# Kernel tuning notes

Hardware: AMD Instinct MI355X
Metric: run time of the kernel (lower is better)

The kernel has to match this reference:

```python
import jax, jax.numpy as jnp
import numpy as np

EMBED_DIM = 512
NUM_HEADS = 8
WINDOW = 64
FFN_RATIO = 4


def _mha(q_in, kv_in, w_in, b_in, w_out, b_out, n_heads, mask=None):
    # Faithful torch.nn.MultiheadAttention (batch_first) with packed in_proj.
    b, sq, d = q_in.shape
    sk = kv_in.shape[1]
    hd = d // n_heads
    wq, wk, wv = jnp.split(w_in, 3, axis=0)   # each [d, d]
    bq, bk, bv = jnp.split(b_in, 3, axis=0)
    q = (q_in @ wq.T + bq).reshape(b, sq, n_heads, hd).transpose(0, 2, 1, 3)
    k = (kv_in @ wk.T + bk).reshape(b, sk, n_heads, hd).transpose(0, 2, 1, 3)
    v = (kv_in @ wv.T + bv).reshape(b, sk, n_heads, hd).transpose(0, 2, 1, 3)
    scores = jnp.einsum('bhqd,bhkd->bhqk', q, k) / jnp.sqrt(jnp.asarray(hd, q.dtype))
    if mask is not None:
        scores = scores + mask  # additive -inf mask, broadcast over [b, h]
    attn = jax.nn.softmax(scores, axis=-1)
    out = jnp.einsum('bhqk,bhkd->bhqd', attn, v)
    out = out.transpose(0, 2, 1, 3).reshape(b, sq, d)
    return out @ w_out.T + b_out


def _layernorm(x, g, b, eps=1e-5):
    mu = jnp.mean(x, axis=-1, keepdims=True)
    var = jnp.var(x, axis=-1, keepdims=True)
    return (x - mu) * jax.lax.rsqrt(var + eps) * g + b


def _local_causal_mask(p, window, dtype=jnp.float32):
    # row i attends to columns [max(0, i-window), i]
    i = jnp.arange(p)[:, None]
    j = jnp.arange(p)[None, :]
    allowed = (j <= i) & (j >= i - window)
    return jnp.where(allowed, jnp.zeros((), dtype), jnp.asarray(-jnp.inf, dtype))


def setup_inputs() -> dict:
    key = jax.random.key(0)
    ks = jax.random.split(key, 20)
    d, h = EMBED_DIM, EMBED_DIM * FFN_RATIO
    s = 0.02
    return {
        'x': jax.random.normal(ks[0], (64, 512, d), jnp.float32),
        'anchors': jax.random.normal(ks[1], (64, 32, d), jnp.float32),
        'lw_in': jax.random.normal(ks[2], (3 * d, d), jnp.float32) * s,
        'lb_in': jnp.zeros((3 * d,), jnp.float32),
        'lw_out': jax.random.normal(ks[3], (d, d), jnp.float32) * s,
        'lb_out': jnp.zeros((d,), jnp.float32),
        'gw_in': jax.random.normal(ks[4], (3 * d, d), jnp.float32) * s,
        'gb_in': jnp.zeros((3 * d,), jnp.float32),
        'gw_out': jax.random.normal(ks[5], (d, d), jnp.float32) * s,
        'gb_out': jnp.zeros((d,), jnp.float32),
        'w1': jax.random.normal(ks[6], (h, d), jnp.float32) * s,
        'b1': jnp.zeros((h,), jnp.float32),
        'w2': jax.random.normal(ks[7], (d, h), jnp.float32) * s,
        'b2': jnp.zeros((d,), jnp.float32),
        'g1': jnp.ones((d,), jnp.float32),
        'be1': jnp.zeros((d,), jnp.float32),
        'g2': jnp.ones((d,), jnp.float32),
        'be2': jnp.zeros((d,), jnp.float32),
    }


def reference(x, anchors, lw_in, lb_in, lw_out, lb_out, gw_in, gb_in, gw_out, gb_out,
              w1, b1, w2, b2, g1, be1, g2, be2):
    p = x.shape[1]
    mask = _local_causal_mask(p, WINDOW, x.dtype)
    x = x + _mha(x, x, lw_in, lb_in, lw_out, lb_out, NUM_HEADS, mask)
    x = x + _mha(x, anchors, gw_in, gb_in, gw_out, gb_out, NUM_HEADS)
    x = _layernorm(x, g1, be1)
    h = jax.nn.gelu(x @ w1.T + b1, approximate=False)
    ffn = h @ w2.T + b2
    return _layernorm(x + ffn, g2, be2)
```

## Files before the change

kernel.cpp:

```cpp
#include <hip/hip_runtime.h>
#include <cmath>


typedef unsigned short u16;
typedef unsigned int u32;
typedef __bf16 bf16_t;
typedef bf16_t bf16x8 __attribute__((ext_vector_type(8)));
typedef float f32x4 __attribute__((ext_vector_type(4)));

#define DEV __device__ __forceinline__
#define MFMA16(a, b, c) __builtin_amdgcn_mfma_f32_16x16x32_bf16(a, b, c, 0, 0, 0)
#define SBAR() __builtin_amdgcn_sched_barrier(0)

DEV u16 f2b(float f) {
  u32 u = __float_as_uint(f);
  u32 r = u + 0x7fffu + ((u >> 16) & 1u);
  return (u16)(r >> 16);
}
DEV float b2f(u16 b) { return __uint_as_float(((u32)b) << 16); }

DEV float gelu_erf(float x) {
  float y = x * 0.70710678118654752f;
  float ay = fabsf(y);
  float t = __builtin_amdgcn_rcpf(1.0f + 0.3275911f * ay);
  float p = t * (0.254829592f +
            t * (-0.284496736f +
            t * (1.421413741f +
            t * (-1.453152027f + t * 1.061405429f))));
  float e = 1.0f - p * __expf(-y * y);
  float erfv = (y < 0.f) ? -e : e;
  return 0.5f * x * (1.0f + erfv);
}

DEV void g2l16(const void* g, void* l) {
  __builtin_amdgcn_global_load_lds((const __attribute__((address_space(1))) void*)g,
                                   (__attribute__((address_space(3))) void*)l,
                                   16, 0, 0);
}

__global__ __launch_bounds__(256) void conv1(const float* __restrict__ s,
                                             u16* __restrict__ d) {
  size_t idx = ((size_t)blockIdx.x * 256 + threadIdx.x) * 8;
  float4 a = *(const float4*)(s + idx);
  float4 b = *(const float4*)(s + idx + 4);
  float v[8] = {a.x, a.y, a.z, a.w, b.x, b.y, b.z, b.w};
  union { u16 q[8]; uint4 u; } pk;
#pragma unroll
  for (int i = 0; i < 8; ++i) pk.q[i] = f2b(v[i]);
  *(uint4*)(d + idx) = pk.u;
}

template <bool GELU, bool RES32, bool RESB, bool OUT32, bool OUTB>
__global__ __launch_bounds__(512, 4) void gemm128(
    const u16* __restrict__ A, const u16* __restrict__ B,
    const float* __restrict__ bias, const float* __restrict__ res32,
    const u16* __restrict__ resb, float* __restrict__ out32,
    u16* __restrict__ outb, int M, int N, int K) {
  __shared__ __align__(16) char smem[73728];
  const int tid = threadIdx.x;
  const int lane = tid & 63, wv = tid >> 6;
  const int warp_m = wv >> 2, warp_n = wv & 3;
  const int lrow = lane & 15, quad = lane >> 4;

  int idx = blockIdx.x;
  {
    const int nwg = gridDim.x;
    if (nwg >= 8) {
      const int q = nwg >> 3, r = nwg & 7;
      const int xcd = idx & 7, rk = idx >> 3;
      idx = (xcd < r ? xcd * (q + 1) : r * (q + 1) + (xcd - r) * q) + rk;
    }
  }
  const int nx = N >> 8;
  const int m0 = (idx / nx) * 128, n0 = (idx % nx) * 256;

  const int srow = tid >> 2;
  const int scol = (((tid & 3) ^ ((tid >> 3) & 3)) << 4);
  const int sdst = tid * 16;
  const int cs = (quad * 16) ^ (((lrow >> 1) & 3) << 4);
  const int rdA = warp_m * 4096 + lrow * 64 + cs;
  const int rdB = warp_n * 4096 + lrow * 64 + cs;

  const int nt = K >> 5;

  auto stage3 = [&](int kt, int slot) {
    const char* ga = (const char*)A + (((size_t)(m0 + srow) * K + kt * 32) << 1) + scol;
    g2l16(ga, smem + slot * 8192 + sdst);
    const char* gb = (const char*)B + (((size_t)(n0 + srow) * K + kt * 32) << 1) + scol;
    char* lb = smem + 24576 + slot * 16384 + sdst;
    g2l16(gb, lb);
    g2l16(gb + ((size_t)K << 8), lb + 8192);
  };

  f32x4 acc[4][4];
  f32x4 zero4 = {0.f, 0.f, 0.f, 0.f};
#pragma unroll
  for (int a = 0; a < 4; ++a)
#pragma unroll
    for (int b = 0; b < 4; ++b) acc[a][b] = zero4;

  stage3(0, 0);
  stage3(1, 1);
  SBAR();
  asm volatile("s_waitcnt vmcnt(3)" ::: "memory");
  asm volatile("s_barrier" ::: "memory");
  SBAR();

  int c0s = 0, c2s = 2;
  for (int kt = 0; kt < nt; ++kt) {
    const char* cA = smem + c0s * 8192;
    const char* cB = smem + 24576 + c0s * 16384;
    bf16x8 afr[4], bfr[4];
#pragma unroll
    for (int m = 0; m < 4; ++m) afr[m] = *(const bf16x8*)(cA + rdA + m * 1024);
#pragma unroll
    for (int n = 0; n < 4; ++n) bfr[n] = *(const bf16x8*)(cB + rdB + n * 1024);
    const int kt2 = (kt + 2 < nt) ? kt + 2 : nt - 1;
    stage3(kt2, c2s);
    SBAR();
    asm volatile("s_barrier" ::: "memory");
    asm volatile("s_waitcnt lgkmcnt(0)" ::: "memory");
    SBAR();
    __builtin_amdgcn_s_setprio(1);
#pragma unroll
    for (int m = 0; m < 4; ++m)
#pragma unroll
      for (int n = 0; n < 4; ++n)
        acc[m][n] = MFMA16(afr[m], bfr[n], acc[m][n]);
    __builtin_amdgcn_s_setprio(0);
    SBAR();
    asm volatile("s_waitcnt vmcnt(3)" ::: "memory");
    asm volatile("s_barrier" ::: "memory");
    SBAR();
    c0s = (c0s == 2) ? 0 : c0s + 1;
    c2s = (c2s == 2) ? 0 : c2s + 1;
  }

  asm volatile("s_waitcnt vmcnt(0)" ::: "memory");
  __syncthreads();

  float* cw = (float*)(smem + (size_t)wv * 4352);
  const int row16 = lane >> 2;
  const int c0 = (lane & 3) * 16;
  const int gcb = n0 + warp_n * 64 + c0;
  float bias16[16];
#pragma unroll
  for (int t = 0; t < 4; ++t) {
    float4 b4 = *(const float4*)(bias + gcb + t * 4);
    bias16[t * 4 + 0] = b4.x; bias16[t * 4 + 1] = b4.y;
    bias16[t * 4 + 2] = b4.z; bias16[t * 4 + 3] = b4.w;
  }

#pragma unroll
  for (int fm = 0; fm < 4; ++fm) {
#pragma unroll
    for (int fn = 0; fn < 4; ++fn)
#pragma unroll
      for (int r = 0; r < 4; ++r)
        cw[(quad * 4 + r) * 68 + fn * 16 + lrow] = acc[fm][fn][r];
    const int grow = m0 + warp_m * 64 + fm * 16 + row16;
    const size_t gbase = (size_t)grow * N + gcb;
    const float* crp = &cw[row16 * 68 + c0];
    float v[16];
#pragma unroll
    for (int t = 0; t < 4; ++t) {
      f32x4 q = *(const f32x4*)(crp + t * 4);
      v[t * 4 + 0] = q[0] + bias16[t * 4 + 0];
      v[t * 4 + 1] = q[1] + bias16[t * 4 + 1];
      v[t * 4 + 2] = q[2] + bias16[t * 4 + 2];
      v[t * 4 + 3] = q[3] + bias16[t * 4 + 3];
    }
    if (RES32) {
#pragma unroll
      for (int t = 0; t < 4; ++t) {
        float4 rr = *(const float4*)(res32 + gbase + t * 4);
        v[t * 4 + 0] += rr.x; v[t * 4 + 1] += rr.y;
        v[t * 4 + 2] += rr.z; v[t * 4 + 3] += rr.w;
      }
    }
    if (RESB) {
#pragma unroll
      for (int t = 0; t < 2; ++t) {
        union { u16 q[8]; uint4 u; } rb;
        rb.u = *(const uint4*)(resb + gbase + t * 8);
#pragma unroll
        for (int j = 0; j < 8; ++j) v[t * 8 + j] += b2f(rb.q[j]);
      }
    }
    if (GELU) {
#pragma unroll
      for (int e = 0; e < 16; ++e) v[e] = gelu_erf(v[e]);
    }
    if (OUT32) {
#pragma unroll
      for (int t = 0; t < 4; ++t) {
        float4 w4 = {v[t * 4 + 0], v[t * 4 + 1], v[t * 4 + 2], v[t * 4 + 3]};
        *(float4*)(out32 + gbase + t * 4) = w4;
      }
    }
    if (OUTB) {
#pragma unroll
      for (int t = 0; t < 2; ++t) {
        union { u16 q[8]; uint4 u; } pk;
#pragma unroll
        for (int j = 0; j < 8; ++j) pk.q[j] = f2b(v[t * 8 + j]);
        *(uint4*)(outb + gbase + t * 8) = pk.u;
      }
    }
  }
}

__global__ __launch_bounds__(256) void local_attn_mfma(const u16* __restrict__ qkv,
                                                       u16* __restrict__ outb) {
  __shared__ u16 vt[64][152];
  __shared__ u16 pb[4][16][104];
  const int tid = threadIdx.x;
  const int lane = tid & 63, w = tid >> 6;
  const int c = lane & 15, quad = lane >> 4;
  const int bx = blockIdx.x;
  const int qb = bx & 7, h = (bx >> 3) & 7, bb = bx >> 6;
  const int i0 = qb * 64;
  const int hc = h * 64;
  const size_t rbase = (size_t)bb * 512;

  {
    int r = tid >> 1;
    int d0 = (tid & 1) * 32;
    int key = i0 - 64 + r;
    if (key < 0) key = 0;
    if (key > 511) key = 511;
    const u16* Vr = qkv + (rbase + key) * 1536 + 1024 + hc + d0;
#pragma unroll
    for (int g = 0; g < 4; ++g) {
      union { u16 q[8]; uint4 u; } vv;
      vv.u = *(const uint4*)(Vr + g * 8);
#pragma unroll
      for (int j = 0; j < 8; ++j) vt[d0 + g * 8 + j][r] = vv.q[j];
    }
    if (tid < 128) {
      int r2 = 128 + (tid >> 3);
      int d2 = (tid & 7) * 8;
      int key2 = i0 - 64 + r2;
      if (key2 < 0) key2 = 0;
      if (key2 > 511) key2 = 511;
      const u16* Vr2 = qkv + (rbase + key2) * 1536 + 1024 + hc + d2;
      union { u16 q[8]; uint4 u; } vv2;
      vv2.u = *(const uint4*)Vr2;
#pragma unroll
      for (int j = 0; j < 8; ++j) vt[d2 + j][r2] = vv2.q[j];
    }
  }
  __syncthreads();

  const int i0w = i0 + 16 * w;
  const int kg0 = i0w - 64;

  bf16x8 qf0, qf1;
  {
    const u16* Qr = qkv + (rbase + i0w + c) * 1536 + hc + quad * 8;
    qf0 = *(const bf16x8*)Qr;
    qf1 = *(const bf16x8*)(Qr + 32);
  }

  f32x4 s[5];
#pragma unroll
  for (int kb = 0; kb < 5; ++kb) {
    int key = kg0 + kb * 16 + c; if (key < 0) key = 0;
    const u16* Kr = qkv + (rbase + key) * 1536 + 512 + hc + quad * 8;
    bf16x8 k0 = *(const bf16x8*)Kr;
    bf16x8 k1 = *(const bf16x8*)(Kr + 32);
    f32x4 z = {0.f, 0.f, 0.f, 0.f};
    z = __builtin_amdgcn_mfma_f32_16x16x32_bf16(qf0, k0, z, 0, 0, 0);
    s[kb] = __builtin_amdgcn_mfma_f32_16x16x32_bf16(qf1, k1, z, 0, 0, 0);
  }

  float mx[4];
#pragma unroll
  for (int r = 0; r < 4; ++r) {
    int row = quad * 4 + r;
    float m = -1e30f;
#pragma unroll
    for (int kb = 0; kb < 5; ++kb) {
      float v = s[kb][r] * 0.125f;
      int key = kg0 + kb * 16 + c;
      bool ok = key >= 0;
      if (kb == 0) ok = ok && (c >= row);
      if (kb == 4) ok = ok && (c <= row);
      v = ok ? v : -1e30f;
      s[kb][r] = v;
      m = fmaxf(m, v);
    }
    mx[r] = m;
  }
#pragma unroll
  for (int o = 1; o <= 8; o <<= 1)
#pragma unroll
    for (int r = 0; r < 4; ++r) mx[r] = fmaxf(mx[r], __shfl_xor(mx[r], o));

  float l[4] = {0.f, 0.f, 0.f, 0.f};
#pragma unroll
  for (int kb = 0; kb < 5; ++kb)
#pragma unroll
    for (int r = 0; r < 4; ++r) {
      u16 pq = f2b(__expf(s[kb][r] - mx[r]));
      l[r] += b2f(pq);
      pb[w][quad * 4 + r][kb * 16 + c] = pq;
    }
#pragma unroll
  for (int r = 0; r < 4; ++r) pb[w][quad * 4 + r][80 + c] = 0;
#pragma unroll
  for (int o = 1; o <= 8; o <<= 1)
#pragma unroll
    for (int r = 0; r < 4; ++r) l[r] += __shfl_xor(l[r], o);
  float inv[4];
#pragma unroll
  for (int r = 0; r < 4; ++r) inv[r] = 1.f / l[r];

  f32x4 o4[4];
#pragma unroll
  for (int nb = 0; nb < 4; ++nb) o4[nb] = f32x4{0.f, 0.f, 0.f, 0.f};
#pragma unroll
  for (int kt = 0; kt < 3; ++kt) {
    bf16x8 pa = *(const bf16x8*)&pb[w][c][kt * 32 + quad * 8];
#pragma unroll
    for (int nb = 0; nb < 4; ++nb) {
      bf16x8 vb = *(const bf16x8*)&vt[nb * 16 + c][16 * w + kt * 32 + quad * 8];
      o4[nb] = __builtin_amdgcn_mfma_f32_16x16x32_bf16(pa, vb, o4[nb], 0, 0, 0);
    }
  }
#pragma unroll
  for (int nb = 0; nb < 4; ++nb)
#pragma unroll
    for (int r = 0; r < 4; ++r) {
      int seq = i0w + quad * 4 + r;
      outb[(rbase + seq) * 512 + hc + nb * 16 + c] = f2b(o4[nb][r] * inv[r]);
    }
}

__global__ __launch_bounds__(256) void global_attn_mfma(const u16* __restrict__ qg,
                                                        const u16* __restrict__ kvg,
                                                        u16* __restrict__ outb) {
  __shared__ u16 vt[64][40];
  __shared__ u16 pb[4][16][40];
  const int tid = threadIdx.x;
  const int lane = tid & 63, w = tid >> 6;
  const int c = lane & 15, quad = lane >> 4;
  const int bx = blockIdx.x;
  const int qb = bx & 7, h = (bx >> 3) & 7, bb = bx >> 6;
  const int i0 = qb * 64;
  const int hc = h * 64;
  const size_t rbase = (size_t)bb * 512;

  {
    int r = tid >> 3;
    int d0 = (tid & 7) * 8;
    const u16* Vr = kvg + ((size_t)bb * 32 + r) * 1024 + 512 + hc + d0;
    union { u16 q[8]; uint4 u; } vv;
    vv.u = *(const uint4*)Vr;
#pragma unroll
    for (int j = 0; j < 8; ++j) vt[d0 + j][r] = vv.q[j];
  }
  __syncthreads();

  const int i0w = i0 + 16 * w;
  bf16x8 qf0, qf1;
  {
    const u16* Qr = qg + (rbase + i0w + c) * 512 + hc + quad * 8;
    qf0 = *(const bf16x8*)Qr;
    qf1 = *(const bf16x8*)(Qr + 32);
  }
  f32x4 s[2];
#pragma unroll
  for (int kb = 0; kb < 2; ++kb) {
    const u16* Kr = kvg + ((size_t)bb * 32 + kb * 16 + c) * 1024 + hc + quad * 8;
    bf16x8 k0 = *(const bf16x8*)Kr;
    bf16x8 k1 = *(const bf16x8*)(Kr + 32);
    f32x4 z = {0.f, 0.f, 0.f, 0.f};
    z = __builtin_amdgcn_mfma_f32_16x16x32_bf16(qf0, k0, z, 0, 0, 0);
    s[kb] = __builtin_amdgcn_mfma_f32_16x16x32_bf16(qf1, k1, z, 0, 0, 0);
  }
  float mx[4];
#pragma unroll
  for (int r = 0; r < 4; ++r)
    mx[r] = fmaxf(s[0][r] * 0.125f, s[1][r] * 0.125f);
#pragma unroll
  for (int o = 1; o <= 8; o <<= 1)
#pragma unroll
    for (int r = 0; r < 4; ++r) mx[r] = fmaxf(mx[r], __shfl_xor(mx[r], o));
  float l[4] = {0.f, 0.f, 0.f, 0.f};
#pragma unroll
  for (int kb = 0; kb < 2; ++kb)
#pragma unroll
    for (int r = 0; r < 4; ++r) {
      u16 pq = f2b(__expf(s[kb][r] * 0.125f - mx[r]));
      l[r] += b2f(pq);
      pb[w][quad * 4 + r][kb * 16 + c] = pq;
    }
#pragma unroll
  for (int o = 1; o <= 8; o <<= 1)
#pragma unroll
    for (int r = 0; r < 4; ++r) l[r] += __shfl_xor(l[r], o);
  float inv[4];
#pragma unroll
  for (int r = 0; r < 4; ++r) inv[r] = 1.f / l[r];

  f32x4 o4[4];
#pragma unroll
  for (int nb = 0; nb < 4; ++nb) o4[nb] = f32x4{0.f, 0.f, 0.f, 0.f};
  bf16x8 pa = *(const bf16x8*)&pb[w][c][quad * 8];
#pragma unroll
  for (int nb = 0; nb < 4; ++nb) {
    bf16x8 vb = *(const bf16x8*)&vt[nb * 16 + c][quad * 8];
    o4[nb] = __builtin_amdgcn_mfma_f32_16x16x32_bf16(pa, vb, o4[nb], 0, 0, 0);
  }
#pragma unroll
  for (int nb = 0; nb < 4; ++nb)
#pragma unroll
    for (int r = 0; r < 4; ++r) {
      int seq = i0w + quad * 4 + r;
      outb[(rbase + seq) * 512 + hc + nb * 16 + c] = f2b(o4[nb][r] * inv[r]);
    }
}

__global__ __launch_bounds__(256) void ln_b2b(const u16* __restrict__ in,
                                              const float* __restrict__ gg,
                                              const float* __restrict__ bb,
                                              u16* __restrict__ outb) {
  const int lane = threadIdx.x & 63;
  const size_t row = (size_t)blockIdx.x * 4 + (threadIdx.x >> 6);
  union { u16 q[8]; uint4 u; } pk;
  pk.u = *(const uint4*)(in + row * 512 + lane * 8);
  float v[8];
#pragma unroll
  for (int e = 0; e < 8; ++e) v[e] = b2f(pk.q[e]);
  float sm = 0.f, sq = 0.f;
#pragma unroll
  for (int e = 0; e < 8; ++e) { sm += v[e]; sq += v[e] * v[e]; }
#pragma unroll
  for (int o = 32; o; o >>= 1) { sm += __shfl_xor(sm, o); sq += __shfl_xor(sq, o); }
  float mean = sm * (1.0f / 512.0f);
  float var = sq * (1.0f / 512.0f) - mean * mean;
  float rs = rsqrtf(var + 1e-5f);
  float4 ga = *(const float4*)(gg + lane * 8);
  float4 gb = *(const float4*)(gg + lane * 8 + 4);
  float4 ba = *(const float4*)(bb + lane * 8);
  float4 bbv = *(const float4*)(bb + lane * 8 + 4);
  float gv[8] = {ga.x, ga.y, ga.z, ga.w, gb.x, gb.y, gb.z, gb.w};
  float bv[8] = {ba.x, ba.y, ba.z, ba.w, bbv.x, bbv.y, bbv.z, bbv.w};
  union { u16 q[8]; uint4 u; } po;
#pragma unroll
  for (int e = 0; e < 8; ++e) po.q[e] = f2b((v[e] - mean) * rs * gv[e] + bv[e]);
  *(uint4*)(outb + row * 512 + lane * 8) = po.u;
}

__global__ __launch_bounds__(256) void ln_f2f(const float* __restrict__ in,
                                              const float* __restrict__ gg,
                                              const float* __restrict__ bb,
                                              float* __restrict__ out) {
  const int lane = threadIdx.x & 63;
  const size_t row = (size_t)blockIdx.x * 4 + (threadIdx.x >> 6);
  const float* p = in + row * 512 + lane * 8;
  float4 a = *(const float4*)p;
  float4 b = *(const float4*)(p + 4);
  float v[8] = {a.x, a.y, a.z, a.w, b.x, b.y, b.z, b.w};
  float sm = 0.f, sq = 0.f;
#pragma unroll
  for (int e = 0; e < 8; ++e) { sm += v[e]; sq += v[e] * v[e]; }
#pragma unroll
  for (int o = 32; o; o >>= 1) { sm += __shfl_xor(sm, o); sq += __shfl_xor(sq, o); }
  float mean = sm * (1.0f / 512.0f);
  float var = sq * (1.0f / 512.0f) - mean * mean;
  float rs = rsqrtf(var + 1e-5f);
  float4 ga = *(const float4*)(gg + lane * 8);
  float4 gb = *(const float4*)(gg + lane * 8 + 4);
  float4 ba = *(const float4*)(bb + lane * 8);
  float4 bbv = *(const float4*)(bb + lane * 8 + 4);
  float gv[8] = {ga.x, ga.y, ga.z, ga.w, gb.x, gb.y, gb.z, gb.w};
  float bv[8] = {ba.x, ba.y, ba.z, ba.w, bbv.x, bbv.y, bbv.z, bbv.w};
  float r[8];
#pragma unroll
  for (int e = 0; e < 8; ++e) r[e] = (v[e] - mean) * rs * gv[e] + bv[e];
  float4 r1 = {r[0], r[1], r[2], r[3]};
  float4 r2 = {r[4], r[5], r[6], r[7]};
  *(float4*)(out + row * 512 + lane * 8) = r1;
  *(float4*)(out + row * 512 + lane * 8 + 4) = r2;
}

extern "C" void kernel_launch(void* const* d_in, const int* in_sizes, int n_in,
                              void* d_out, int out_size, void* d_ws, size_t ws_size,
                              hipStream_t stream) {
  const float* x      = (const float*)d_in[0];
  const float* anchors= (const float*)d_in[1];
  const float* lw_in  = (const float*)d_in[2];
  const float* lb_in  = (const float*)d_in[3];
  const float* lw_out = (const float*)d_in[4];
  const float* lb_out = (const float*)d_in[5];
  const float* gw_in  = (const float*)d_in[6];
  const float* gb_in  = (const float*)d_in[7];
  const float* gw_out = (const float*)d_in[8];
  const float* gb_out = (const float*)d_in[9];
  const float* w1     = (const float*)d_in[10];
  const float* b1     = (const float*)d_in[11];
  const float* w2     = (const float*)d_in[12];
  const float* b2     = (const float*)d_in[13];
  const float* g1     = (const float*)d_in[14];
  const float* be1    = (const float*)d_in[15];
  const float* g2     = (const float*)d_in[16];
  const float* be2    = (const float*)d_in[17];
  (void)in_sizes; (void)n_in; (void)out_size;
  float* out = (float*)d_out;

  char* ws = (char*)d_ws;
  size_t o = 0;
  auto nxt = [&](size_t bytes) { char* p = ws + o; o += bytes; return p; };
  u16* lwib = (u16*)nxt((size_t)1536 * 512 * 2);
  u16* lwob = (u16*)nxt((size_t)512 * 512 * 2);
  u16* gwib = (u16*)nxt((size_t)1536 * 512 * 2);
  u16* gwob = (u16*)nxt((size_t)512 * 512 * 2);
  u16* w1b  = (u16*)nxt((size_t)2048 * 512 * 2);
  u16* w2b  = (u16*)nxt((size_t)512 * 2048 * 2);
  u16* ab   = (u16*)nxt((size_t)2048 * 512 * 2);
  u16* kvgb = (u16*)nxt((size_t)2048 * 1024 * 2);
  const size_t wbytes = o;

  int nc = 1;
  while (wbytes + (size_t)(32768 / nc) * 6144 > ws_size && nc < 32) nc <<= 1;
  const int Mc = 32768 / nc;
  const int nBat = Mc / 512;
  const int mb7 = Mc >> 7;
  u16* BIGb = (u16*)nxt((size_t)Mc * 4096);
  u16* Pb   = (u16*)nxt((size_t)Mc * 1024);
  u16* Qb   = (u16*)nxt((size_t)Mc * 1024);
  u16* Sb   = BIGb + (size_t)Mc * 1536;

  conv1<<<384, 256, 0, stream>>>(lw_in, lwib);
  conv1<<<128, 256, 0, stream>>>(lw_out, lwob);
  conv1<<<384, 256, 0, stream>>>(gw_in, gwib);
  conv1<<<128, 256, 0, stream>>>(gw_out, gwob);
  conv1<<<512, 256, 0, stream>>>(w1, w1b);
  conv1<<<512, 256, 0, stream>>>(w2, w2b);
  conv1<<<512, 256, 0, stream>>>(anchors, ab);
  gemm128<false, false, false, false, true><<<16 * 4, 512, 0, stream>>>(
      ab, gwib + 512 * 512, gb_in + 512, nullptr, nullptr, nullptr, kvgb, 2048, 1024, 512);

  for (int ck = 0; ck < nc; ++ck) {
    const size_t r0 = (size_t)ck * Mc;
    const float* xck = x + r0 * 512;
    conv1<<<Mc / 4, 256, 0, stream>>>(xck, Pb);
    gemm128<false, false, false, false, true><<<mb7 * 6, 512, 0, stream>>>(
        Pb, lwib, lb_in, nullptr, nullptr, nullptr, BIGb, Mc, 1536, 512);
    local_attn_mfma<<<nBat * 64, 256, 0, stream>>>(BIGb, Sb);
    gemm128<false, true, false, false, true><<<mb7 * 2, 512, 0, stream>>>(
        Sb, lwob, lb_out, xck, nullptr, nullptr, Qb, Mc, 512, 512);
    gemm128<false, false, false, false, true><<<mb7 * 2, 512, 0, stream>>>(
        Qb, gwib, gb_in, nullptr, nullptr, nullptr, Pb, Mc, 512, 512);
    global_attn_mfma<<<nBat * 64, 256, 0, stream>>>(Pb, kvgb + (r0 / 512) * 32 * 1024, Sb);
    gemm128<false, false, true, false, true><<<mb7 * 2, 512, 0, stream>>>(
        Sb, gwob, gb_out, nullptr, Qb, nullptr, Pb, Mc, 512, 512);
    ln_b2b<<<Mc / 4, 256, 0, stream>>>(Pb, g1, be1, Qb);
    gemm128<true, false, false, false, true><<<mb7 * 8, 512, 0, stream>>>(
        Qb, w1b, b1, nullptr, nullptr, nullptr, BIGb, Mc, 2048, 512);
    gemm128<false, false, true, true, false><<<mb7 * 2, 512, 0, stream>>>(
        BIGb, w2b, b2, nullptr, Qb, out + r0 * 512, nullptr, Mc, 512, 2048);
    ln_f2f<<<Mc / 4, 256, 0, stream>>>(out + r0 * 512, g2, be2, out + r0 * 512);
  }
}
```

Baseline: 629.0 us.

## Widen GEMM tile to 128x512 with 1024 threads and fuse LayerNorm epilogues

Replaces the 128x256 GEMM with a 128x512 tile run by 16 waves, so a block covers a full 512-wide row. The two LayerNorm kernels can then be fused into the GEMM epilogues through a cross-wave shared-memory reduction of row sums. The A tile is staged in 64-wide K chunks while B keeps a three-slot ring. This removes two launches and their extra activation round trips and improves B reuse per A load. The cost is one block per CU with large LDS, fewer blocks per grid, and the residual buffer Qb being read and written in place by the same GEMM.

```diff
diff --git a/kernel.cpp b/kernel.cpp
--- a/kernel.cpp
+++ b/kernel.cpp
@@ -50,16 +50,17 @@
   *(uint4*)(d + idx) = pk.u;
 }
 
-template <bool GELU, bool RES32, bool RESB, bool OUT32, bool OUTB>
-__global__ __launch_bounds__(512, 4) void gemm128(
+template <bool GELU, bool RES32, bool RESB, bool LN, bool OUT32, bool OUTB>
+__global__ __launch_bounds__(1024, 1) void gemmW(
     const u16* __restrict__ A, const u16* __restrict__ B,
     const float* __restrict__ bias, const float* __restrict__ res32,
-    const u16* __restrict__ resb, float* __restrict__ out32,
+    const u16* __restrict__ resb, const float* __restrict__ lnG,
+    const float* __restrict__ lnB, float* __restrict__ out32,
     u16* __restrict__ outb, int M, int N, int K) {
-  __shared__ __align__(16) char smem[73728];
+  __shared__ __align__(16) char smem[147456];
   const int tid = threadIdx.x;
   const int lane = tid & 63, wv = tid >> 6;
-  const int warp_m = wv >> 2, warp_n = wv & 3;
+  const int wm = wv >> 3, wn = wv & 7;
   const int lrow = lane & 15, quad = lane >> 4;
 
   int idx = blockIdx.x;
@@ -71,26 +72,30 @@
       idx = (xcd < r ? xcd * (q + 1) : r * (q + 1) + (xcd - r) * q) + rk;
     }
   }
-  const int nx = N >> 8;
-  const int m0 = (idx / nx) * 128, n0 = (idx % nx) * 256;
-
-  const int srow = tid >> 2;
-  const int scol = (((tid & 3) ^ ((tid >> 3) & 3)) << 4);
+  const int nx = N >> 9;
+  const int m0 = (idx / nx) * 128, n0 = (idx % nx) * 512;
+
+  const int c0q = quad ^ (lrow & 3);
+  const int hbit = (lrow >> 2) & 1;
+  int aOffE[4], aOffO[4], bOff[4];
+#pragma unroll
+  for (int m = 0; m < 4; ++m) {
+    const int rb = (wm * 64 + m * 16 + lrow) * 128;
+    aOffE[m] = rb + (c0q + hbit * 4) * 16;
+    aOffO[m] = rb + (c0q + (1 - hbit) * 4) * 16;
+  }
+#pragma unroll
+  for (int n = 0; n < 4; ++n)
+    bOff[n] = (wn * 64 + n * 16 + lrow) * 64 + ((quad ^ ((lrow >> 1) & 3)) * 16);
+
+  const int lB = (tid & 3) ^ ((tid >> 3) & 3);
+  const char* Bsrc0 = (const char*)B + (((size_t)(n0 + (tid >> 2)) * K + lB * 8) << 1);
+  const char* Bsrc1 = (const char*)B + (((size_t)(n0 + 256 + (tid >> 2)) * K + lB * 8) << 1);
+  const int lA = (tid & 7) ^ ((tid >> 3) & 7);
+  const char* Asrc = (const char*)A + (((size_t)(m0 + (tid >> 3)) * K + lA * 8) << 1);
+
+  const int nt = K >> 5, ntp = nt >> 1;
   const int sdst = tid * 16;
-  const int cs = (quad * 16) ^ (((lrow >> 1) & 3) << 4);
-  const int rdA = warp_m * 4096 + lrow * 64 + cs;
-  const int rdB = warp_n * 4096 + lrow * 64 + cs;
-
-  const int nt = K >> 5;
-
-  auto stage3 = [&](int kt, int slot) {
-    const char* ga = (const char*)A + (((size_t)(m0 + srow) * K + kt * 32) << 1) + scol;
-    g2l16(ga, smem + slot * 8192 + sdst);
-    const char* gb = (const char*)B + (((size_t)(n0 + srow) * K + kt * 32) << 1) + scol;
-    char* lb = smem + 24576 + slot * 16384 + sdst;
-    g2l16(gb, lb);
-    g2l16(gb + ((size_t)K << 8), lb + 8192);
-  };
 
   f32x4 acc[4][4];
   f32x4 zero4 = {0.f, 0.f, 0.f, 0.f};
@@ -99,50 +104,68 @@
 #pragma unroll
     for (int b = 0; b < 4; ++b) acc[a][b] = zero4;
 
-  stage3(0, 0);
-  stage3(1, 1);
+  g2l16(Asrc, smem + sdst);
+  g2l16(Asrc + 128, smem + 16384 + sdst);
+  g2l16(Bsrc0, smem + 49152 + sdst);
+  g2l16(Bsrc1, smem + 49152 + 16384 + sdst);
+  g2l16(Bsrc0 + 64, smem + 49152 + 32768 + sdst);
+  g2l16(Bsrc1 + 64, smem + 49152 + 32768 + 16384 + sdst);
   SBAR();
-  asm volatile("s_waitcnt vmcnt(3)" ::: "memory");
+  asm volatile("s_waitcnt vmcnt(2)" ::: "memory");
   asm volatile("s_barrier" ::: "memory");
   SBAR();
 
-  int c0s = 0, c2s = 2;
-  for (int kt = 0; kt < nt; ++kt) {
-    const char* cA = smem + c0s * 8192;
-    const char* cB = smem + 24576 + c0s * 16384;
-    bf16x8 afr[4], bfr[4];
-#pragma unroll
-    for (int m = 0; m < 4; ++m) afr[m] = *(const bf16x8*)(cA + rdA + m * 1024);
-#pragma unroll
-    for (int n = 0; n < 4; ++n) bfr[n] = *(const bf16x8*)(cB + rdB + n * 1024);
-    const int kt2 = (kt + 2 < nt) ? kt + 2 : nt - 1;
-    stage3(kt2, c2s);
-    SBAR();
-    asm volatile("s_barrier" ::: "memory");
-    asm volatile("s_waitcnt lgkmcnt(0)" ::: "memory");
-    SBAR();
-    __builtin_amdgcn_s_setprio(1);
-#pragma unroll
-    for (int m = 0; m < 4; ++m)
+  int sB0 = 0, sB2 = 2, pA = 0, pA2 = 2;
+  for (int tp = 0; tp < ntp; ++tp) {
+#pragma unroll
+    for (int half = 0; half < 2; ++half) {
+      const int t = tp * 2 + half;
+      const char* Ab = smem + pA * 16384;
+      const char* Bb = smem + 49152 + sB0 * 32768;
+      bf16x8 afr[4], bfr[4];
+#pragma unroll
+      for (int m = 0; m < 4; ++m)
+        afr[m] = *(const bf16x8*)(Ab + (half ? aOffO[m] : aOffE[m]));
 #pragma unroll
       for (int n = 0; n < 4; ++n)
-        acc[m][n] = MFMA16(afr[m], bfr[n], acc[m][n]);
-    __builtin_amdgcn_s_setprio(0);
-    SBAR();
-    asm volatile("s_waitcnt vmcnt(3)" ::: "memory");
-    asm volatile("s_barrier" ::: "memory");
-    SBAR();
-    c0s = (c0s == 2) ? 0 : c0s + 1;
-    c2s = (c2s == 2) ? 0 : c2s + 1;
+        bfr[n] = *(const bf16x8*)(Bb + bOff[n]);
+      const int ktB = (t + 2 < nt) ? t + 2 : nt - 1;
+      char* bd = smem + 49152 + sB2 * 32768;
+      g2l16(Bsrc0 + ((size_t)ktB << 6), bd + sdst);
+      g2l16(Bsrc1 + ((size_t)ktB << 6), bd + 16384 + sdst);
+      if (half == 0) {
+        const int p2 = (tp + 2 < ntp) ? tp + 2 : ntp - 1;
+        g2l16(Asrc + ((size_t)p2 << 7), smem + pA2 * 16384 + sdst);
+      }
+      SBAR();
+      asm volatile("s_waitcnt lgkmcnt(0)" ::: "memory");
+      SBAR();
+      __builtin_amdgcn_s_setprio(1);
+#pragma unroll
+      for (int m = 0; m < 4; ++m)
+#pragma unroll
+        for (int n = 0; n < 4; ++n)
+          acc[m][n] = MFMA16(afr[m], bfr[n], acc[m][n]);
+      __builtin_amdgcn_s_setprio(0);
+      SBAR();
+      asm volatile("s_waitcnt vmcnt(3)" ::: "memory");
+      asm volatile("s_barrier" ::: "memory");
+      SBAR();
+      sB0 = (sB0 == 2) ? 0 : sB0 + 1;
+      sB2 = (sB2 == 2) ? 0 : sB2 + 1;
+    }
+    pA = (pA == 2) ? 0 : pA + 1;
+    pA2 = (pA2 == 2) ? 0 : pA2 + 1;
   }
 
   asm volatile("s_waitcnt vmcnt(0)" ::: "memory");
   __syncthreads();
 
   float* cw = (float*)(smem + (size_t)wv * 4352);
+  float* red = (float*)(smem + 131072);
   const int row16 = lane >> 2;
   const int c0 = (lane & 3) * 16;
-  const int gcb = n0 + warp_n * 64 + c0;
+  const int gcb = n0 + wn * 64 + c0;
   float bias16[16];
 #pragma unroll
   for (int t = 0; t < 4; ++t) {
@@ -151,6 +174,7 @@
     bias16[t * 4 + 2] = b4.z; bias16[t * 4 + 3] = b4.w;
   }
 
+  float vv[4][16];
 #pragma unroll
   for (int fm = 0; fm < 4; ++fm) {
 #pragma unroll
@@ -158,7 +182,7 @@
 #pragma unroll
       for (int r = 0; r < 4; ++r)
         cw[(quad * 4 + r) * 68 + fn * 16 + lrow] = acc[fm][fn][r];
-    const int grow = m0 + warp_m * 64 + fm * 16 + row16;
+    const int grow = m0 + wm * 64 + fm * 16 + row16;
     const size_t gbase = (size_t)grow * N + gcb;
     const float* crp = &cw[row16 * 68 + c0];
     float v[16];
@@ -191,20 +215,86 @@
 #pragma unroll
       for (int e = 0; e < 16; ++e) v[e] = gelu_erf(v[e]);
     }
-    if (OUT32) {
+    if (LN) {
+      float s1 = 0.f, s2 = 0.f;
+#pragma unroll
+      for (int e = 0; e < 16; ++e) { s1 += v[e]; s2 += v[e] * v[e]; }
+      s1 += __shfl_xor(s1, 1); s2 += __shfl_xor(s2, 1);
+      s1 += __shfl_xor(s1, 2); s2 += __shfl_xor(s2, 2);
+      if ((lane & 3) == 0) {
+        const int lr = wm * 64 + fm * 16 + row16;
+        red[(lr * 8 + wn) * 2 + 0] = s1;
+        red[(lr * 8 + wn) * 2 + 1] = s2;
+      }
+#pragma unroll
+      for (int e = 0; e < 16; ++e) vv[fm][e] = v[e];
+    } else {
+      if (OUT32) {
+#pragma unroll
+        for (int t = 0; t < 4; ++t) {
+          float4 w4 = {v[t * 4 + 0], v[t * 4 + 1], v[t * 4 + 2], v[t * 4 + 3]};
+          *(float4*)(out32 + gbase + t * 4) = w4;
+        }
+      }
+      if (OUTB) {
+#pragma unroll
+        for (int t = 0; t < 2; ++t) {
+          union { u16 q[8]; uint4 u; } pk;
+#pragma unroll
+          for (int j = 0; j < 8; ++j) pk.q[j] = f2b(v[t * 8 + j]);
+          *(uint4*)(outb + gbase + t * 8) = pk.u;
+        }
+      }
+    }
+  }
+
+  if (LN) {
+    __syncthreads();
+    float g16[16], b16[16];
+#pragma unroll
+    for (int t = 0; t < 4; ++t) {
+      float4 gg = *(const float4*)(lnG + gcb + t * 4);
+      float4 bb = *(const float4*)(lnB + gcb + t * 4);
+      g16[t * 4 + 0] = gg.x; g16[t * 4 + 1] = gg.y;
+      g16[t * 4 + 2] = gg.z; g16[t * 4 + 3] = gg.w;
+      b16[t * 4 + 0] = bb.x; b16[t * 4 + 1] = bb.y;
+      b16[t * 4 + 2] = bb.z; b16[t * 4 + 3] = bb.w;
+    }
+#pragma unroll
+    for (int fm = 0; fm < 4; ++fm) {
+      const int lr = wm * 64 + fm * 16 + row16;
+      const float* rp = &red[lr * 16];
+      float s1 = 0.f, s2 = 0.f;
 #pragma unroll
       for (int t = 0; t < 4; ++t) {
-        float4 w4 = {v[t * 4 + 0], v[t * 4 + 1], v[t * 4 + 2], v[t * 4 + 3]};
-        *(float4*)(out32 + gbase + t * 4) = w4;
-      }
-    }
-    if (OUTB) {
-#pragma unroll
-      for (int t = 0; t < 2; ++t) {
-        union { u16 q[8]; uint4 u; } pk;
-#pragma unroll
-        for (int j = 0; j < 8; ++j) pk.q[j] = f2b(v[t * 8 + j]);
-        *(uint4*)(outb + gbase + t * 8) = pk.u;
+        f32x4 q = *(const f32x4*)(rp + t * 4);
+        s1 += q[0] + q[2];
+        s2 += q[1] + q[3];
+      }
+      const float mean = s1 * (1.0f / 512.0f);
+      const float var = s2 * (1.0f / 512.0f) - mean * mean;
+      const float rs = rsqrtf(var + 1e-5f);
+      const int grow = m0 + wm * 64 + fm * 16 + row16;
+      const size_t gbase = (size_t)grow * N + gcb;
+      float o[16];
+#pragma unroll
+      for (int e = 0; e < 16; ++e)
+        o[e] = (vv[fm][e] - mean) * rs * g16[e] + b16[e];
+      if (OUT32) {
+#pragma unroll
+        for (int t = 0; t < 4; ++t) {
+          float4 w4 = {o[t * 4 + 0], o[t * 4 + 1], o[t * 4 + 2], o[t * 4 + 3]};
+          *(float4*)(out32 + gbase + t * 4) = w4;
+        }
+      }
+      if (OUTB) {
+#pragma unroll
+        for (int t = 0; t < 2; ++t) {
+          union { u16 q[8]; uint4 u; } pk;
+#pragma unroll
+          for (int j = 0; j < 8; ++j) pk.q[j] = f2b(o[t * 8 + j]);
+          *(uint4*)(outb + gbase + t * 8) = pk.u;
+        }
       }
     }
   }
@@ -420,70 +510,6 @@
       int seq = i0w + quad * 4 + r;
       outb[(rbase + seq) * 512 + hc + nb * 16 + c] = f2b(o4[nb][r] * inv[r]);
     }
-}
-
-__global__ __launch_bounds__(256) void ln_b2b(const u16* __restrict__ in,
-                                              const float* __restrict__ gg,
-                                              const float* __restrict__ bb,
-                                              u16* __restrict__ outb) {
-  const int lane = threadIdx.x & 63;
-  const size_t row = (size_t)blockIdx.x * 4 + (threadIdx.x >> 6);
-  union { u16 q[8]; uint4 u; } pk;
-  pk.u = *(const uint4*)(in + row * 512 + lane * 8);
-  float v[8];
-#pragma unroll
-  for (int e = 0; e < 8; ++e) v[e] = b2f(pk.q[e]);
-  float sm = 0.f, sq = 0.f;
-#pragma unroll
-  for (int e = 0; e < 8; ++e) { sm += v[e]; sq += v[e] * v[e]; }
-#pragma unroll
-  for (int o = 32; o; o >>= 1) { sm += __shfl_xor(sm, o); sq += __shfl_xor(sq, o); }
-  float mean = sm * (1.0f / 512.0f);
-  float var = sq * (1.0f / 512.0f) - mean * mean;
-  float rs = rsqrtf(var + 1e-5f);
-  float4 ga = *(const float4*)(gg + lane * 8);
-  float4 gb = *(const float4*)(gg + lane * 8 + 4);
-  float4 ba = *(const float4*)(bb + lane * 8);
-  float4 bbv = *(const float4*)(bb + lane * 8 + 4);
-  float gv[8] = {ga.x, ga.y, ga.z, ga.w, gb.x, gb.y, gb.z, gb.w};
-  float bv[8] = {ba.x, ba.y, ba.z, ba.w, bbv.x, bbv.y, bbv.z, bbv.w};
-  union { u16 q[8]; uint4 u; } po;
-#pragma unroll
-  for (int e = 0; e < 8; ++e) po.q[e] = f2b((v[e] - mean) * rs * gv[e] + bv[e]);
-  *(uint4*)(outb + row * 512 + lane * 8) = po.u;
-}
-
-__global__ __launch_bounds__(256) void ln_f2f(const float* __restrict__ in,
-                                              const float* __restrict__ gg,
-                                              const float* __restrict__ bb,
-                                              float* __restrict__ out) {
-  const int lane = threadIdx.x & 63;
-  const size_t row = (size_t)blockIdx.x * 4 + (threadIdx.x >> 6);
-  const float* p = in + row * 512 + lane * 8;
-  float4 a = *(const float4*)p;
-  float4 b = *(const float4*)(p + 4);
-  float v[8] = {a.x, a.y, a.z, a.w, b.x, b.y, b.z, b.w};
-  float sm = 0.f, sq = 0.f;
-#pragma unroll
-  for (int e = 0; e < 8; ++e) { sm += v[e]; sq += v[e] * v[e]; }
-#pragma unroll
-  for (int o = 32; o; o >>= 1) { sm += __shfl_xor(sm, o); sq += __shfl_xor(sq, o); }
-  float mean = sm * (1.0f / 512.0f);
-  float var = sq * (1.0f / 512.0f) - mean * mean;
-  float rs = rsqrtf(var + 1e-5f);
-  float4 ga = *(const float4*)(gg + lane * 8);
-  float4 gb = *(const float4*)(gg + lane * 8 + 4);
-  float4 ba = *(const float4*)(bb + lane * 8);
-  float4 bbv = *(const float4*)(bb + lane * 8 + 4);
-  float gv[8] = {ga.x, ga.y, ga.z, ga.w, gb.x, gb.y, gb.z, gb.w};
-  float bv[8] = {ba.x, ba.y, ba.z, ba.w, bbv.x, bbv.y, bbv.z, bbv.w};
-  float r[8];
-#pragma unroll
-  for (int e = 0; e < 8; ++e) r[e] = (v[e] - mean) * rs * gv[e] + bv[e];
-  float4 r1 = {r[0], r[1], r[2], r[3]};
-  float4 r2 = {r[4], r[5], r[6], r[7]};
-  *(float4*)(out + row * 512 + lane * 8) = r1;
-  *(float4*)(out + row * 512 + lane * 8 + 4) = r2;
 }
 
 extern "C" void kernel_launch(void* const* d_in, const int* in_sizes, int n_in,
@@ -527,7 +553,7 @@
   while (wbytes + (size_t)(32768 / nc) * 6144 > ws_size && nc < 32) nc <<= 1;
   const int Mc = 32768 / nc;
   const int nBat = Mc / 512;
-  const int mb7 = Mc >> 7;
+  const int mbW = Mc >> 7;
   u16* BIGb = (u16*)nxt((size_t)Mc * 4096);
   u16* Pb   = (u16*)nxt((size_t)Mc * 1024);
   u16* Qb   = (u16*)nxt((size_t)Mc * 1024);
@@ -540,28 +566,33 @@
   conv1<<<512, 256, 0, stream>>>(w1, w1b);
   conv1<<<512, 256, 0, stream>>>(w2, w2b);
   conv1<<<512, 256, 0, stream>>>(anchors, ab);
-  gemm128<false, false, false, false, true><<<16 * 4, 512, 0, stream>>>(
-      ab, gwib + 512 * 512, gb_in + 512, nullptr, nullptr, nullptr, kvgb, 2048, 1024, 512);
+  gemmW<false, false, false, false, false, true><<<16 * 2, 1024, 0, stream>>>(
+      ab, gwib + 512 * 512, gb_in + 512, nullptr, nullptr, nullptr, nullptr,
+      nullptr, kvgb, 2048, 1024, 512);
 
   for (int ck = 0; ck < nc; ++ck) {
     const size_t r0 = (size_t)ck * Mc;
     const float* xck = x + r0 * 512;
     conv1<<<Mc / 4, 256, 0, stream>>>(xck, Pb);
-    gemm128<false, false, false, false, true><<<mb7 * 6, 512, 0, stream>>>(
-        Pb, lwib, lb_in, nullptr, nullptr, nullptr, BIGb, Mc, 1536, 512);
+    gemmW<false, false, false, false, false, true><<<mbW * 3, 1024, 0, stream>>>(
+        Pb, lwib, lb_in, nullptr, nullptr, nullptr, nullptr,
+        nullptr, BIGb, Mc, 1536, 512);
     local_attn_mfma<<<nBat * 64, 256, 0, stream>>>(BIGb, Sb);
-    gemm128<false, true, false, false, true><<<mb7 * 2, 512, 0, stream>>>(
-        Sb, lwob, lb_out, xck, nullptr, nullptr, Qb, Mc, 512, 512);
-    gemm128<false, false, false, false, true><<<mb7 * 2, 512, 0, stream>>>(
-        Qb, gwib, gb_in, nullptr, nullptr, nullptr, Pb, Mc, 512, 512);
+    gemmW<false, true, false, false, false, true><<<mbW, 1024, 0, stream>>>(
+        Sb, lwob, lb_out, xck, nullptr, nullptr, nullptr,
+        nullptr, Qb, Mc, 512, 512);
+    gemmW<false, false, false, false, false, true><<<mbW, 1024, 0, stream>>>(
+        Qb, gwib, gb_in, nullptr, nullptr, nullptr, nullptr,
+        nullptr, Pb, Mc, 512, 512);
     global_attn_mfma<<<nBat * 64, 256, 0, stream>>>(Pb, kvgb + (r0 / 512) * 32 * 1024, Sb);
-    gemm128<false, false, true, false, true><<<mb7 * 2, 512, 0, stream>>>(
-        Sb, gwob, gb_out, nullptr, Qb, nullptr, Pb, Mc, 512, 512);
-    ln_b2b<<<Mc / 4, 256, 0, stream>>>(Pb, g1, be1, Qb);
-    gemm128<true, false, false, false, true><<<mb7 * 8, 512, 0, stream>>>(
-        Qb, w1b, b1, nullptr, nullptr, nullptr, BIGb, Mc, 2048, 512);
-    gemm128<false, false, true, true, false><<<mb7 * 2, 512, 0, stream>>>(
-        BIGb, w2b, b2, nullptr, Qb, out + r0 * 512, nullptr, Mc, 512, 2048);
-    ln_f2f<<<Mc / 4, 256, 0, stream>>>(out + r0 * 512, g2, be2, out + r0 * 512);
-  }
-}
+    gemmW<false, false, true, true, false, true><<<mbW, 1024, 0, stream>>>(
+        Sb, gwob, gb_out, nullptr, Qb, g1, be1,
+        nullptr, Qb, Mc, 512, 512);
+    gemmW<true, false, false, false, false, true><<<mbW * 4, 1024, 0, stream>>>(
+        Qb, w1b, b1, nullptr, nullptr, nullptr, nullptr,
+        nullptr, BIGb, Mc, 2048, 512);
+    gemmW<false, false, true, true, true, false><<<mbW, 1024, 0, stream>>>(
+        BIGb, w2b, b2, nullptr, Qb, g2, be2,
+        out + r0 * 512, nullptr, Mc, 512, 2048);
+  }
+}
```

Result: faster. 615.7 us (-2.1%).
